# Optimization experiments

Measured on AMD Instinct MI355X. Metric: run time of the kernel, lower is better.

## Reference

```python
import jax, jax.numpy as jnp
import numpy as np

BS, SEQ = 32, 48
VOCAB, H, IMG_F = 32529, 512, 4096
EPS = 1e-5


def setup_inputs() -> dict:
    key = jax.random.key(0)
    ks = jax.random.split(key, 24)
    stdv = 1.0 / np.sqrt(H)
    u = lambda k, shp, s=stdv: jax.random.uniform(k, shp, jnp.float32, -s, s)
    inp = {
        'img': jax.random.normal(ks[0], (BS, IMG_F), jnp.float32),
        'x': jax.random.randint(ks[1], (BS, SEQ), 0, VOCAB),
        # CNN (all convs are kernel-size-1 -> plain linears)
        'w1': u(ks[2], (2048, IMG_F)), 'b1': u(ks[3], (2048,)),
        'g1': jnp.ones((2048,)), 'be1': jnp.zeros((2048,)),
        'w2': u(ks[4], (1024, 2048)), 'b2': u(ks[5], (1024,)),
        'g2': jnp.ones((1024,)), 'be2': jnp.zeros((1024,)),
        'w3': u(ks[6], (H, 1024)), 'b3': u(ks[7], (H,)),
        'g3': jnp.ones((H,)), 'be3': jnp.zeros((H,)),
        # LSTM gates stacked in order i, f, g(c), o
        'U': u(ks[8], (H, 4 * H)),
        'V': u(ks[9], (H, 4 * H)),
        'bg': u(ks[10], (4 * H,)),
        'emb': u(ks[11], (VOCAB, H)),
        'Wout': u(ks[12], (H, VOCAB)),
        'bout': u(ks[13], (VOCAB,)),
    }
    return inp


def _bn(h, g, b):
    # BatchNorm1d in training mode over batch dim (spatial length is 1)
    mu = h.mean(0)
    v = jnp.var(h, 0)
    return g * (h - mu) * jax.lax.rsqrt(v + EPS) + b


def _cnn(img, w1, b1, g1, be1, w2, b2, g2, be2, w3, b3, g3, be3):
    h = jax.nn.relu(_bn(img @ w1.T + b1, g1, be1))
    h = jax.nn.relu(_bn(h @ w2.T + b2, g2, be2))
    h = jax.nn.relu(_bn(h @ w3.T + b3, g3, be3))
    return h  # [bs, 512]


def _lstm(feat, xe, U, V, bg):
    bs = feat.shape[0]
    h = jnp.zeros((bs, H), feat.dtype)
    c = jnp.zeros((bs, H), feat.dtype)

    def gates(z, c):
        z = z.reshape(bs, 4, H)
        i = jax.nn.sigmoid(z[:, 0])
        f = jax.nn.sigmoid(z[:, 1])
        g = jnp.tanh(z[:, 2])
        o = jax.nn.sigmoid(z[:, 3])
        c = f * c + i * g
        return o * jnp.tanh(c), c

    # image step: feat is added identically to every gate pre-activation
    z0 = feat[:, None, :].repeat(4, 1).reshape(bs, 4 * H) + h @ V + bg
    h, c = gates(z0, c)

    # precompute all input projections in one GEMM: [seq, bs, 4H]
    xU = jnp.einsum('bsh,hk->sbk', xe, U)

    def step(carry, xu):
        h, c = carry
        h, c = gates(xu + h @ V + bg, c)
        return (h, c), h

    (h, c), hs = jax.lax.scan(step, (h, c), xU)
    return hs.transpose(1, 0, 2), h, c  # [bs, seq, H]


def reference(img, x, w1, b1, g1, be1, w2, b2, g2, be2, w3, b3, g3, be3,
              U, V, bg, emb, Wout, bout):
    feat = _cnn(img, w1, b1, g1, be1, w2, b2, g2, be2, w3, b3, g3, be3)
    xe = emb[x]  # [bs, seq, H]
    hs, h, c = _lstm(feat, xe, U, V, bg)
    logits = hs @ Wout + bout  # [bs, seq, vocab]
    seq_pred = jax.nn.softmax(logits, axis=2)
    return seq_pred, (h, c)
```

## Files before the change

kernel.cpp:

```cpp
#include <hip/hip_runtime.h>
#include <stdint.h>

#define BS 32
#define SEQ 48
#define VOCAB 32529
#define HD 512
#define IMG_F 4096
#define EPS 1e-5f

typedef __attribute__((ext_vector_type(8))) short short8;
typedef __attribute__((ext_vector_type(4))) float f32x4;

#define MFMA(a, b, c) __builtin_amdgcn_mfma_f32_16x16x32_bf16(a, b, c, 0, 0, 0)

static __device__ __forceinline__ unsigned short f2bf(float v) {
  union { float f; unsigned u; } c; c.f = v;
  unsigned r = (c.u + 0x7FFFu + ((c.u >> 16) & 1u)) >> 16;
  return (unsigned short)r;
}
static __device__ __forceinline__ float bf2f(unsigned short h) {
  union { unsigned u; float f; } c; c.u = ((unsigned)h) << 16; return c.f;
}
static __device__ __forceinline__ float sigf(float x) {
  x = fminf(fmaxf(x, -30.f), 30.f);
  return 1.f / (1.f + __expf(-x));
}
static __device__ __forceinline__ float tanh_(float x) {
  float t = __expf(fminf(fmaxf(2.f * x, -30.f), 30.f));
  return (t - 1.f) / (t + 1.f);
}

__global__ __launch_bounds__(256) void k_gather(const float* __restrict__ emb,
                                                const int* __restrict__ x,
                                                unsigned short* __restrict__ xh,
                                                unsigned short* __restrict__ xl) {
  int idx = blockIdx.x * 256 + threadIdx.x;
  int m = idx >> 7;
  int k4 = (idx & 127) << 2;
  int t = m >> 5, b = m & 31;
  int row = x[b * SEQ + t];
  float4 v = *(const float4*)(emb + (size_t)row * HD + k4);
  float vv[4] = {v.x, v.y, v.z, v.w};
  unsigned short h_[4], l_[4];
#pragma unroll
  for (int i = 0; i < 4; ++i) {
    h_[i] = f2bf(vv[i]);
    l_[i] = f2bf(vv[i] - bf2f(h_[i]));
  }
  ushort4 hq = {h_[0], h_[1], h_[2], h_[3]};
  ushort4 lq = {l_[0], l_[1], l_[2], l_[3]};
  *(ushort4*)(xh + (size_t)m * HD + k4) = hq;
  *(ushort4*)(xl + (size_t)m * HD + k4) = lq;
}

__global__ __launch_bounds__(256) void k_pack(const float* __restrict__ W,
                                              unsigned short* __restrict__ Ph,
                                              unsigned short* __restrict__ Pl) {
  int f = blockIdx.x * 256 + threadIdx.x;
  int lane = f & 63;
  int kk = (f >> 6) & 15;
  int n16 = f >> 10;
  int c = n16 * 16 + (lane & 15);
  int k0 = kk * 32 + (lane >> 4) * 8;
  short8 oh, ol;
#pragma unroll
  for (int i = 0; i < 8; ++i) {
    float v = W[(size_t)(k0 + i) * 2048 + c];
    unsigned short hb = f2bf(v);
    oh[i] = (short)hb;
    ol[i] = (short)f2bf(v - bf2f(hb));
  }
  *(short8*)(Ph + (size_t)f * 8) = oh;
  *(short8*)(Pl + (size_t)f * 8) = ol;
}

template <int INF, int OUTF>
__global__ __launch_bounds__(256) void k_cnn(const float* __restrict__ in,
                                             const float* __restrict__ W,
                                             const float* __restrict__ gamma,
                                             const float* __restrict__ beta,
                                             float* __restrict__ out) {
  int tid = threadIdx.x;
  int b = tid & 31;
  int o = blockIdx.x * 8 + (tid >> 5);
  const float4* ip = (const float4*)(in + (size_t)b * INF);
  const float4* wp = (const float4*)(W + (size_t)o * INF);
  float a0 = 0, a1 = 0, a2 = 0, a3 = 0;
#pragma unroll 4
  for (int k = 0; k < INF / 4; ++k) {
    float4 a = ip[k], w = wp[k];
    a0 = fmaf(a.x, w.x, a0);
    a1 = fmaf(a.y, w.y, a1);
    a2 = fmaf(a.z, w.z, a2);
    a3 = fmaf(a.w, w.w, a3);
  }
  float pre = (a0 + a1) + (a2 + a3);
  float s = pre, q = pre * pre;
#pragma unroll
  for (int mk = 16; mk >= 1; mk >>= 1) {
    s += __shfl_xor(s, mk);
    q += __shfl_xor(q, mk);
  }
  float mu = s * (1.f / 32.f);
  float var = q * (1.f / 32.f) - mu * mu;
  float y = gamma[o] * (pre - mu) * rsqrtf(var + EPS) + beta[o];
  out[(size_t)b * OUTF + o] = fmaxf(y, 0.f);
}

__global__ __launch_bounds__(256) void k_xu(const unsigned short* __restrict__ xh,
                                            const unsigned short* __restrict__ xl,
                                            const unsigned short* __restrict__ Uh,
                                            const unsigned short* __restrict__ Ul,
                                            const float* __restrict__ bg,
                                            float* __restrict__ zx) {
  int mb = blockIdx.x;
  int nb = blockIdx.y;
  int w = threadIdx.x >> 6, l = threadIdx.x & 63;
  int lr = l & 15, lg = l >> 4;
  f32x4 acc[2][2] = {};
#pragma unroll 2
  for (int kk = 0; kk < 16; ++kk) {
    short8 ah[2], al[2];
#pragma unroll
    for (int m = 0; m < 2; ++m) {
      size_t ao = (size_t)(mb * 32 + m * 16 + lr) * HD + kk * 32 + lg * 8;
      ah[m] = *(const short8*)(xh + ao);
      al[m] = *(const short8*)(xl + ao);
    }
#pragma unroll
    for (int n = 0; n < 2; ++n) {
      int n16 = nb * 8 + w * 2 + n;
      size_t bo = ((size_t)(n16 * 16 + kk) * 64 + l) * 8;
      short8 bh = *(const short8*)(Uh + bo);
      short8 bl = *(const short8*)(Ul + bo);
#pragma unroll
      for (int m = 0; m < 2; ++m) {
        acc[m][n] = MFMA(ah[m], bh, acc[m][n]);
        acc[m][n] = MFMA(al[m], bh, acc[m][n]);
        acc[m][n] = MFMA(ah[m], bl, acc[m][n]);
      }
    }
  }
#pragma unroll
  for (int m = 0; m < 2; ++m)
#pragma unroll
    for (int n = 0; n < 2; ++n) {
      int col = (nb * 8 + w * 2 + n) * 16 + lr;
#pragma unroll
      for (int r = 0; r < 4; ++r) {
        int row = mb * 32 + m * 16 + lg * 4 + r;
        zx[(size_t)row * 2048 + col] = acc[m][n][r] + bg[col];
      }
    }
}

__global__ __launch_bounds__(256) void k_step0(const float* __restrict__ feat,
                                               const float* __restrict__ bg,
                                               float* __restrict__ hbuf, float* __restrict__ cbuf,
                                               unsigned short* __restrict__ hh,
                                               unsigned short* __restrict__ hl) {
  int idx = blockIdx.x * 256 + threadIdx.x;
  int j = idx & 511;
  float fv = feat[idx];
  float ig = sigf(fv + bg[j]);
  float gg = tanh_(fv + bg[1024 + j]);
  float og = sigf(fv + bg[1536 + j]);
  float c = ig * gg;
  float h = og * tanh_(c);
  cbuf[idx] = c;
  hbuf[idx] = h;
  unsigned short hb = f2bf(h);
  hh[idx] = hb;
  hl[idx] = f2bf(h - bf2f(hb));
}

__global__ __launch_bounds__(256) void k_step(int t,
    const unsigned short* __restrict__ hih, const unsigned short* __restrict__ hil,
    unsigned short* __restrict__ hoh, unsigned short* __restrict__ hol,
    const unsigned short* __restrict__ Vh, const unsigned short* __restrict__ Vl,
    const float* __restrict__ zx, float* __restrict__ cbuf, float* __restrict__ hbuf,
    unsigned short* __restrict__ hsb) {
  __shared__ float zsh[4][16][17];
  int nb = blockIdx.x & 31;
  int mh = blockIdx.x >> 5;
  int w = threadIdx.x >> 6, l = threadIdx.x & 63;
  int lr = l & 15, lg = l >> 4;
  f32x4 acc = {};
  int n16 = w * 32 + nb;
#pragma unroll 4
  for (int kk = 0; kk < 16; ++kk) {
    size_t ao = (size_t)(mh * 16 + lr) * HD + kk * 32 + lg * 8;
    short8 ah = *(const short8*)(hih + ao);
    short8 al = *(const short8*)(hil + ao);
    size_t bo = ((size_t)(n16 * 16 + kk) * 64 + l) * 8;
    short8 bh = *(const short8*)(Vh + bo);
    short8 bl = *(const short8*)(Vl + bo);
    acc = MFMA(ah, bh, acc);
    acc = MFMA(al, bh, acc);
    acc = MFMA(ah, bl, acc);
  }
#pragma unroll
  for (int r = 0; r < 4; ++r) zsh[w][lg * 4 + r][lr] = acc[r];
  __syncthreads();
  int bl_ = threadIdx.x >> 4;
  int j = threadIdx.x & 15;
  int b = mh * 16 + bl_;
  int col = nb * 16 + j;
  const float* zr = zx + (size_t)(t * 32 + b) * 2048;
  float zi = zsh[0][bl_][j] + zr[col];
  float zf = zsh[1][bl_][j] + zr[512 + col];
  float zg = zsh[2][bl_][j] + zr[1024 + col];
  float zo = zsh[3][bl_][j] + zr[1536 + col];
  float ig = sigf(zi), fg = sigf(zf), gg = tanh_(zg), og = sigf(zo);
  int ci = b * HD + col;
  float c = fg * cbuf[ci] + ig * gg;
  float h = og * tanh_(c);
  cbuf[ci] = c;
  hbuf[ci] = h;
  unsigned short hb = f2bf(h);
  hoh[ci] = hb;
  hol[ci] = f2bf(h - bf2f(hb));
  hsb[((size_t)b * SEQ + t) * HD + col] = hb;
}

template <int MODE>
__global__ __launch_bounds__(256) void k_out(const unsigned short* __restrict__ hsb,
                                             const float* __restrict__ Wout,
                                             const float* __restrict__ bout,
                                             float* __restrict__ rowsum,
                                             float* __restrict__ dst) {
  __shared__ __align__(16) unsigned short Bl[4][64][8];
  int nb = blockIdx.x, mb = blockIdx.y;
  int n0 = nb * 64;
  int tid = threadIdx.x;
  int w = tid >> 6, l = tid & 63, lr = l & 15, lg = l >> 4;
  int mrow0 = mb * 256 + w * 64;
  f32x4 acc[4][4] = {};
  int kl = tid >> 3;
  int nl = (tid & 7) * 8;
  int nsub = nl >> 4;
  int lbase = (nl & 15) | ((kl >> 3) << 4);
  int ifr = kl & 7;
  for (int kk = 0; kk < 16; ++kk) {
    float v[8];
    const float* src = Wout + (size_t)(kk * 32 + kl) * VOCAB + n0 + nl;
#pragma unroll
    for (int i = 0; i < 8; ++i) {
      int gv = n0 + nl + i;
      v[i] = (gv < VOCAB) ? src[i] : 0.f;
    }
    __syncthreads();
#pragma unroll
    for (int i = 0; i < 8; ++i) Bl[nsub][lbase + i][ifr] = f2bf(v[i]);
    __syncthreads();
    short8 a[4];
#pragma unroll
    for (int mt = 0; mt < 4; ++mt)
      a[mt] = *(const short8*)(hsb + (size_t)(mrow0 + mt * 16 + lr) * HD + kk * 32 + lg * 8);
#pragma unroll
    for (int nt = 0; nt < 4; ++nt) {
      short8 bf = *(const short8*)(&Bl[nt][l][0]);
#pragma unroll
      for (int mt = 0; mt < 4; ++mt) acc[mt][nt] = MFMA(a[mt], bf, acc[mt][nt]);
    }
  }
#pragma unroll
  for (int mt = 0; mt < 4; ++mt) {
#pragma unroll
    for (int r = 0; r < 4; ++r) {
      int row = mrow0 + mt * 16 + lg * 4 + r;
      float inv = 1.f;
      if (MODE == 1) inv = 1.f / rowsum[row];
      float s = 0.f;
#pragma unroll
      for (int nt = 0; nt < 4; ++nt) {
        int col = n0 + nt * 16 + lr;
        bool valid = col < VOCAB;
        float logit = acc[mt][nt][r] + (valid ? bout[col] : 0.f);
        float e = __expf(logit);
        if (MODE == 0) {
          s += valid ? e : 0.f;
        } else if (MODE == 2) {
          s += valid ? e : 0.f;
          if (valid) dst[(size_t)row * VOCAB + col] = e;
        } else {
          if (valid) dst[(size_t)row * VOCAB + col] = e * inv;
        }
      }
      if (MODE != 1) {
        s += __shfl_xor(s, 1);
        s += __shfl_xor(s, 2);
        s += __shfl_xor(s, 4);
        s += __shfl_xor(s, 8);
        if (lr == 0) atomicAdd(&rowsum[row], s);
      }
    }
  }
}

__global__ __launch_bounds__(256) void k_div(const float* __restrict__ expb,
                                             const float* __restrict__ rowsum,
                                             float* __restrict__ out) {
  unsigned idx = blockIdx.x * 256u + threadIdx.x;
  unsigned row = idx / (unsigned)VOCAB;
  out[idx] = expb[idx] / rowsum[row];
}

extern "C" void kernel_launch(void* const* d_in, const int* in_sizes, int n_in,
                              void* d_out, int out_size, void* d_ws, size_t ws_size,
                              hipStream_t stream) {
  const float* img  = (const float*)d_in[0];
  const int*   x    = (const int*)d_in[1];
  const float* w1   = (const float*)d_in[2];
  const float* g1   = (const float*)d_in[4];
  const float* be1  = (const float*)d_in[5];
  const float* w2   = (const float*)d_in[6];
  const float* g2   = (const float*)d_in[8];
  const float* be2  = (const float*)d_in[9];
  const float* w3   = (const float*)d_in[10];
  const float* g3   = (const float*)d_in[12];
  const float* be3  = (const float*)d_in[13];
  const float* U    = (const float*)d_in[14];
  const float* V    = (const float*)d_in[15];
  const float* bg   = (const float*)d_in[16];
  const float* emb  = (const float*)d_in[17];
  const float* Wout = (const float*)d_in[18];
  const float* bout = (const float*)d_in[19];

  char* ws = (char*)d_ws;
  size_t off = 0;
  auto alloc = [&](size_t bytes) -> void* {
    void* p = ws + off;
    off = (off + bytes + 255) & ~(size_t)255;
    return p;
  };
  float* zx = (float*)alloc((size_t)48 * 32 * 2048 * 4);
  unsigned short* xh = (unsigned short*)alloc((size_t)1536 * 512 * 2);
  unsigned short* xl = (unsigned short*)alloc((size_t)1536 * 512 * 2);
  unsigned short* Uh = (unsigned short*)alloc((size_t)512 * 2048 * 2);
  unsigned short* Ul = (unsigned short*)alloc((size_t)512 * 2048 * 2);
  unsigned short* Vh = (unsigned short*)alloc((size_t)512 * 2048 * 2);
  unsigned short* Vl = (unsigned short*)alloc((size_t)512 * 2048 * 2);
  unsigned short* hAh = (unsigned short*)alloc(32 * 512 * 2);
  unsigned short* hAl = (unsigned short*)alloc(32 * 512 * 2);
  unsigned short* hBh = (unsigned short*)alloc(32 * 512 * 2);
  unsigned short* hBl = (unsigned short*)alloc(32 * 512 * 2);
  float* hbuf = (float*)alloc(32 * 512 * 4);
  float* cbuf = (float*)alloc(32 * 512 * 4);
  unsigned short* hsb = (unsigned short*)alloc((size_t)1536 * 512 * 2);
  float* feat = (float*)alloc(32 * 512 * 4);
  float* h1 = (float*)alloc(32 * 2048 * 4);
  float* h2 = (float*)alloc(32 * 1024 * 4);
  float* rowsum = (float*)alloc(1536 * 4);
  size_t base = off;
  float* expb = (float*)(ws + base);
  const size_t EXPB = (size_t)49964544 * 4;
  bool onepass = (ws_size >= base + EXPB);

  float* out = (float*)d_out;

  k_gather<<<dim3(768), dim3(256), 0, stream>>>(emb, x, xh, xl);
  k_pack<<<dim3(512), dim3(256), 0, stream>>>(U, Uh, Ul);
  k_pack<<<dim3(512), dim3(256), 0, stream>>>(V, Vh, Vl);
  k_cnn<4096, 2048><<<dim3(256), dim3(256), 0, stream>>>(img, w1, g1, be1, h1);
  k_cnn<2048, 1024><<<dim3(128), dim3(256), 0, stream>>>(h1, w2, g2, be2, h2);
  k_cnn<1024, 512><<<dim3(64), dim3(256), 0, stream>>>(h2, w3, g3, be3, feat);
  k_xu<<<dim3(48, 16), dim3(256), 0, stream>>>(xh, xl, Uh, Ul, bg, zx);
  k_step0<<<dim3(64), dim3(256), 0, stream>>>(feat, bg, hbuf, cbuf, hAh, hAl);
  for (int t = 0; t < 48; ++t) {
    const unsigned short* ih = (t & 1) ? hBh : hAh;
    const unsigned short* il = (t & 1) ? hBl : hAl;
    unsigned short* oh = (t & 1) ? hAh : hBh;
    unsigned short* ol = (t & 1) ? hAl : hBl;
    k_step<<<dim3(64), dim3(256), 0, stream>>>(t, ih, il, oh, ol, Vh, Vl, zx, cbuf, hbuf, hsb);
  }
  hipMemsetAsync(rowsum, 0, 1536 * 4, stream);
  if (onepass) {
    k_out<2><<<dim3(509, 6), dim3(256), 0, stream>>>(hsb, Wout, bout, rowsum, expb);
    k_div<<<dim3(195174), dim3(256), 0, stream>>>(expb, rowsum, out);
  } else {
    k_out<0><<<dim3(509, 6), dim3(256), 0, stream>>>(hsb, Wout, bout, rowsum, out);
    k_out<1><<<dim3(509, 6), dim3(256), 0, stream>>>(hsb, Wout, bout, rowsum, out);
  }
  hipMemcpyAsync(out + 49964544, hbuf, 32 * 512 * 4, hipMemcpyDeviceToDevice, stream);
  hipMemcpyAsync(out + 49964544 + 16384, cbuf, 32 * 512 * 4, hipMemcpyDeviceToDevice, stream);
}
```

Before: 1.502 ms.

## Persistent LSTM kernel with grid barrier, prepacked bf16 Wout, two-pass softmax

Replaces the 48 per-step LSTM launches with one persistent 64-block kernel. It keeps V fragments in registers and synchronises steps with an atomic-counter grid barrier, and writes h/c straight to the output. Wout is prepacked once into an MFMA-ready bf16 layout, so the output GEMM reads B fragments from global memory with no LDS staging or per-tile conversion. The one-pass exp-buffer-plus-divide path is dropped in favour of always running two GEMM passes (sum, then normalise), which recomputes the GEMM but avoids a 200MB intermediate. The grid barrier relies on all 64 blocks being co-resident, and the packing kernel adds its own cost.

```diff
diff --git a/kernel.cpp b/kernel.cpp
--- a/kernel.cpp
+++ b/kernel.cpp
@@ -7,6 +7,7 @@
 #define HD 512
 #define IMG_F 4096
 #define EPS 1e-5f
+#define NPAD16 2040
 
 typedef __attribute__((ext_vector_type(8))) short short8;
 typedef __attribute__((ext_vector_type(4))) float f32x4;
@@ -28,6 +29,17 @@
 static __device__ __forceinline__ float tanh_(float x) {
   float t = __expf(fminf(fmaxf(2.f * x, -30.f), 30.f));
   return (t - 1.f) / (t + 1.f);
+}
+
+static __device__ __forceinline__ void gbar(unsigned* ctr, unsigned target) {
+  __syncthreads();
+  if (threadIdx.x == 0) {
+    __threadfence();
+    atomicAdd(ctr, 1u);
+    while (atomicAdd(ctr, 0u) < target) __builtin_amdgcn_s_sleep(2);
+  }
+  __syncthreads();
+  __threadfence();
 }
 
 __global__ __launch_bounds__(256) void k_gather(const float* __restrict__ emb,
@@ -74,6 +86,23 @@
   *(short8*)(Pl + (size_t)f * 8) = ol;
 }
 
+__global__ __launch_bounds__(256) void k_packw(const float* __restrict__ W,
+                                               unsigned short* __restrict__ P) {
+  int f = blockIdx.x * 256 + threadIdx.x;
+  int lane = f & 63;
+  int kk = (f >> 6) & 15;
+  int n16 = f >> 10;
+  int c = n16 * 16 + (lane & 15);
+  int k0 = kk * 32 + (lane >> 4) * 8;
+  short8 o;
+#pragma unroll
+  for (int i = 0; i < 8; ++i) {
+    float v = (c < VOCAB) ? W[(size_t)(k0 + i) * VOCAB + c] : 0.f;
+    o[i] = (short)f2bf(v);
+  }
+  *(short8*)(P + (size_t)f * 8) = o;
+}
+
 template <int INF, int OUTF>
 __global__ __launch_bounds__(256) void k_cnn(const float* __restrict__ in,
                                              const float* __restrict__ W,
@@ -86,7 +115,7 @@
   const float4* ip = (const float4*)(in + (size_t)b * INF);
   const float4* wp = (const float4*)(W + (size_t)o * INF);
   float a0 = 0, a1 = 0, a2 = 0, a3 = 0;
-#pragma unroll 4
+#pragma unroll 8
   for (int k = 0; k < INF / 4; ++k) {
     float4 a = ip[k], w = wp[k];
     a0 = fmaf(a.x, w.x, a0);
@@ -154,115 +183,111 @@
     }
 }
 
-__global__ __launch_bounds__(256) void k_step0(const float* __restrict__ feat,
-                                               const float* __restrict__ bg,
-                                               float* __restrict__ hbuf, float* __restrict__ cbuf,
-                                               unsigned short* __restrict__ hh,
-                                               unsigned short* __restrict__ hl) {
-  int idx = blockIdx.x * 256 + threadIdx.x;
-  int j = idx & 511;
-  float fv = feat[idx];
-  float ig = sigf(fv + bg[j]);
-  float gg = tanh_(fv + bg[1024 + j]);
-  float og = sigf(fv + bg[1536 + j]);
-  float c = ig * gg;
-  float h = og * tanh_(c);
-  cbuf[idx] = c;
-  hbuf[idx] = h;
-  unsigned short hb = f2bf(h);
-  hh[idx] = hb;
-  hl[idx] = f2bf(h - bf2f(hb));
-}
-
-__global__ __launch_bounds__(256) void k_step(int t,
-    const unsigned short* __restrict__ hih, const unsigned short* __restrict__ hil,
-    unsigned short* __restrict__ hoh, unsigned short* __restrict__ hol,
+__global__ __launch_bounds__(256, 1) void k_lstm(
+    const float* __restrict__ feat, const float* __restrict__ bg,
+    const float* __restrict__ zx,
     const unsigned short* __restrict__ Vh, const unsigned short* __restrict__ Vl,
-    const float* __restrict__ zx, float* __restrict__ cbuf, float* __restrict__ hbuf,
-    unsigned short* __restrict__ hsb) {
+    unsigned short* __restrict__ hAh, unsigned short* __restrict__ hAl,
+    unsigned short* __restrict__ hBh, unsigned short* __restrict__ hBl,
+    unsigned short* __restrict__ hsb, float* __restrict__ hout,
+    float* __restrict__ cout_, unsigned* __restrict__ barctr) {
   __shared__ float zsh[4][16][17];
-  int nb = blockIdx.x & 31;
-  int mh = blockIdx.x >> 5;
-  int w = threadIdx.x >> 6, l = threadIdx.x & 63;
-  int lr = l & 15, lg = l >> 4;
-  f32x4 acc = {};
+  int blk = blockIdx.x;
+  int mh = blk >> 5, nb = blk & 31;
+  int tid = threadIdx.x;
+  int w = tid >> 6, l = tid & 63, lr = l & 15, lg = l >> 4;
   int n16 = w * 32 + nb;
-#pragma unroll 4
+  short8 vh[16], vl[16];
+#pragma unroll
   for (int kk = 0; kk < 16; ++kk) {
-    size_t ao = (size_t)(mh * 16 + lr) * HD + kk * 32 + lg * 8;
-    short8 ah = *(const short8*)(hih + ao);
-    short8 al = *(const short8*)(hil + ao);
     size_t bo = ((size_t)(n16 * 16 + kk) * 64 + l) * 8;
-    short8 bh = *(const short8*)(Vh + bo);
-    short8 bl = *(const short8*)(Vl + bo);
-    acc = MFMA(ah, bh, acc);
-    acc = MFMA(al, bh, acc);
-    acc = MFMA(ah, bl, acc);
-  }
-#pragma unroll
-  for (int r = 0; r < 4; ++r) zsh[w][lg * 4 + r][lr] = acc[r];
-  __syncthreads();
-  int bl_ = threadIdx.x >> 4;
-  int j = threadIdx.x & 15;
-  int b = mh * 16 + bl_;
-  int col = nb * 16 + j;
-  const float* zr = zx + (size_t)(t * 32 + b) * 2048;
-  float zi = zsh[0][bl_][j] + zr[col];
-  float zf = zsh[1][bl_][j] + zr[512 + col];
-  float zg = zsh[2][bl_][j] + zr[1024 + col];
-  float zo = zsh[3][bl_][j] + zr[1536 + col];
-  float ig = sigf(zi), fg = sigf(zf), gg = tanh_(zg), og = sigf(zo);
+    vh[kk] = *(const short8*)(Vh + bo);
+    vl[kk] = *(const short8*)(Vl + bo);
+  }
+  int bl_ = tid >> 4, j = tid & 15;
+  int b = mh * 16 + bl_, col = nb * 16 + j;
   int ci = b * HD + col;
-  float c = fg * cbuf[ci] + ig * gg;
-  float h = og * tanh_(c);
-  cbuf[ci] = c;
-  hbuf[ci] = h;
-  unsigned short hb = f2bf(h);
-  hoh[ci] = hb;
-  hol[ci] = f2bf(h - bf2f(hb));
-  hsb[((size_t)b * SEQ + t) * HD + col] = hb;
+  float fv = feat[ci];
+  float c = sigf(fv + bg[col]) * tanh_(fv + bg[1024 + col]);
+  float h = sigf(fv + bg[1536 + col]) * tanh_(c);
+  {
+    unsigned short hb_ = f2bf(h);
+    hAh[ci] = hb_;
+    hAl[ci] = f2bf(h - bf2f(hb_));
+  }
+  gbar(barctr, 64u);
+  for (int t = 0; t < 48; ++t) {
+    const unsigned short* ih = (t & 1) ? hBh : hAh;
+    const unsigned short* il = (t & 1) ? hBl : hAl;
+    unsigned short* oh = (t & 1) ? hAh : hBh;
+    unsigned short* ol = (t & 1) ? hAl : hBl;
+    const float* zr = zx + ((size_t)t * 32 + b) * 2048 + col;
+    float z0p = zr[0], z1p = zr[512], z2p = zr[1024], z3p = zr[1536];
+    f32x4 acc0 = {}, acc1 = {};
+#pragma unroll
+    for (int kk = 0; kk < 16; ++kk) {
+      size_t ao = (size_t)(mh * 16 + lr) * HD + kk * 32 + lg * 8;
+      short8 ah = *(const short8*)(ih + ao);
+      short8 al = *(const short8*)(il + ao);
+      if (kk & 1) {
+        acc1 = MFMA(ah, vh[kk], acc1);
+        acc1 = MFMA(al, vh[kk], acc1);
+        acc1 = MFMA(ah, vl[kk], acc1);
+      } else {
+        acc0 = MFMA(ah, vh[kk], acc0);
+        acc0 = MFMA(al, vh[kk], acc0);
+        acc0 = MFMA(ah, vl[kk], acc0);
+      }
+    }
+    f32x4 acc;
+#pragma unroll
+    for (int r = 0; r < 4; ++r) acc[r] = acc0[r] + acc1[r];
+#pragma unroll
+    for (int r = 0; r < 4; ++r) zsh[w][lg * 4 + r][lr] = acc[r];
+    __syncthreads();
+    float zi = zsh[0][bl_][j] + z0p;
+    float zf = zsh[1][bl_][j] + z1p;
+    float zg = zsh[2][bl_][j] + z2p;
+    float zo = zsh[3][bl_][j] + z3p;
+    c = sigf(zf) * c + sigf(zi) * tanh_(zg);
+    h = sigf(zo) * tanh_(c);
+    unsigned short hb2 = f2bf(h);
+    oh[ci] = hb2;
+    ol[ci] = f2bf(h - bf2f(hb2));
+    hsb[((size_t)b * SEQ + t) * HD + col] = hb2;
+    if (t < 47) gbar(barctr, 64u * (t + 2));
+  }
+  hout[ci] = h;
+  cout_[ci] = c;
 }
 
 template <int MODE>
-__global__ __launch_bounds__(256) void k_out(const unsigned short* __restrict__ hsb,
-                                             const float* __restrict__ Wout,
+__global__ __launch_bounds__(256) void k_out(const unsigned short* __restrict__ A,
+                                             const unsigned short* __restrict__ B,
                                              const float* __restrict__ bout,
                                              float* __restrict__ rowsum,
                                              float* __restrict__ dst) {
-  __shared__ __align__(16) unsigned short Bl[4][64][8];
-  int nb = blockIdx.x, mb = blockIdx.y;
-  int n0 = nb * 64;
+  int nb = blockIdx.x;
+  int mb = blockIdx.y;
   int tid = threadIdx.x;
   int w = tid >> 6, l = tid & 63, lr = l & 15, lg = l >> 4;
-  int mrow0 = mb * 256 + w * 64;
+  int wr = w >> 1, wc = w & 1;
+  int mrow0 = mb * 128 + wr * 64;
+  int n16_0 = nb * 8 + wc * 4;
   f32x4 acc[4][4] = {};
-  int kl = tid >> 3;
-  int nl = (tid & 7) * 8;
-  int nsub = nl >> 4;
-  int lbase = (nl & 15) | ((kl >> 3) << 4);
-  int ifr = kl & 7;
+#pragma unroll 2
   for (int kk = 0; kk < 16; ++kk) {
-    float v[8];
-    const float* src = Wout + (size_t)(kk * 32 + kl) * VOCAB + n0 + nl;
-#pragma unroll
-    for (int i = 0; i < 8; ++i) {
-      int gv = n0 + nl + i;
-      v[i] = (gv < VOCAB) ? src[i] : 0.f;
-    }
-    __syncthreads();
-#pragma unroll
-    for (int i = 0; i < 8; ++i) Bl[nsub][lbase + i][ifr] = f2bf(v[i]);
-    __syncthreads();
-    short8 a[4];
+    short8 a[4], bf[4];
 #pragma unroll
     for (int mt = 0; mt < 4; ++mt)
-      a[mt] = *(const short8*)(hsb + (size_t)(mrow0 + mt * 16 + lr) * HD + kk * 32 + lg * 8);
-#pragma unroll
-    for (int nt = 0; nt < 4; ++nt) {
-      short8 bf = *(const short8*)(&Bl[nt][l][0]);
-#pragma unroll
-      for (int mt = 0; mt < 4; ++mt) acc[mt][nt] = MFMA(a[mt], bf, acc[mt][nt]);
-    }
+      a[mt] = *(const short8*)(A + (size_t)(mrow0 + mt * 16 + lr) * HD + kk * 32 + lg * 8);
+#pragma unroll
+    for (int nt = 0; nt < 4; ++nt)
+      bf[nt] = *(const short8*)(B + ((size_t)((n16_0 + nt) * 16 + kk) * 64 + l) * 8);
+#pragma unroll
+    for (int nt = 0; nt < 4; ++nt)
+#pragma unroll
+      for (int mt = 0; mt < 4; ++mt) acc[mt][nt] = MFMA(a[mt], bf[nt], acc[mt][nt]);
   }
 #pragma unroll
   for (int mt = 0; mt < 4; ++mt) {
@@ -274,20 +299,16 @@
       float s = 0.f;
 #pragma unroll
       for (int nt = 0; nt < 4; ++nt) {
-        int col = n0 + nt * 16 + lr;
+        int col = (n16_0 + nt) * 16 + lr;
         bool valid = col < VOCAB;
-        float logit = acc[mt][nt][r] + (valid ? bout[col] : 0.f);
-        float e = __expf(logit);
+        float e = __expf(acc[mt][nt][r] + (valid ? bout[col] : 0.f));
         if (MODE == 0) {
           s += valid ? e : 0.f;
-        } else if (MODE == 2) {
-          s += valid ? e : 0.f;
-          if (valid) dst[(size_t)row * VOCAB + col] = e;
         } else {
           if (valid) dst[(size_t)row * VOCAB + col] = e * inv;
         }
       }
-      if (MODE != 1) {
+      if (MODE == 0) {
         s += __shfl_xor(s, 1);
         s += __shfl_xor(s, 2);
         s += __shfl_xor(s, 4);
@@ -296,14 +317,6 @@
       }
     }
   }
-}
-
-__global__ __launch_bounds__(256) void k_div(const float* __restrict__ expb,
-                                             const float* __restrict__ rowsum,
-                                             float* __restrict__ out) {
-  unsigned idx = blockIdx.x * 256u + threadIdx.x;
-  unsigned row = idx / (unsigned)VOCAB;
-  out[idx] = expb[idx] / rowsum[row];
 }
 
 extern "C" void kernel_launch(void* const* d_in, const int* in_sizes, int n_in,
@@ -341,47 +354,34 @@
   unsigned short* Ul = (unsigned short*)alloc((size_t)512 * 2048 * 2);
   unsigned short* Vh = (unsigned short*)alloc((size_t)512 * 2048 * 2);
   unsigned short* Vl = (unsigned short*)alloc((size_t)512 * 2048 * 2);
+  unsigned short* Wp = (unsigned short*)alloc((size_t)NPAD16 * 16 * 64 * 8 * 2);
   unsigned short* hAh = (unsigned short*)alloc(32 * 512 * 2);
   unsigned short* hAl = (unsigned short*)alloc(32 * 512 * 2);
   unsigned short* hBh = (unsigned short*)alloc(32 * 512 * 2);
   unsigned short* hBl = (unsigned short*)alloc(32 * 512 * 2);
-  float* hbuf = (float*)alloc(32 * 512 * 4);
-  float* cbuf = (float*)alloc(32 * 512 * 4);
   unsigned short* hsb = (unsigned short*)alloc((size_t)1536 * 512 * 2);
   float* feat = (float*)alloc(32 * 512 * 4);
   float* h1 = (float*)alloc(32 * 2048 * 4);
   float* h2 = (float*)alloc(32 * 1024 * 4);
   float* rowsum = (float*)alloc(1536 * 4);
-  size_t base = off;
-  float* expb = (float*)(ws + base);
-  const size_t EXPB = (size_t)49964544 * 4;
-  bool onepass = (ws_size >= base + EXPB);
+  unsigned* barctr = (unsigned*)alloc(256);
 
   float* out = (float*)d_out;
+  float* hout = out + 49964544;
+  float* cout_ = out + 49964544 + 16384;
 
   k_gather<<<dim3(768), dim3(256), 0, stream>>>(emb, x, xh, xl);
   k_pack<<<dim3(512), dim3(256), 0, stream>>>(U, Uh, Ul);
   k_pack<<<dim3(512), dim3(256), 0, stream>>>(V, Vh, Vl);
+  k_packw<<<dim3(8160), dim3(256), 0, stream>>>(Wout, Wp);
   k_cnn<4096, 2048><<<dim3(256), dim3(256), 0, stream>>>(img, w1, g1, be1, h1);
   k_cnn<2048, 1024><<<dim3(128), dim3(256), 0, stream>>>(h1, w2, g2, be2, h2);
   k_cnn<1024, 512><<<dim3(64), dim3(256), 0, stream>>>(h2, w3, g3, be3, feat);
   k_xu<<<dim3(48, 16), dim3(256), 0, stream>>>(xh, xl, Uh, Ul, bg, zx);
-  k_step0<<<dim3(64), dim3(256), 0, stream>>>(feat, bg, hbuf, cbuf, hAh, hAl);
-  for (int t = 0; t < 48; ++t) {
-    const unsigned short* ih = (t & 1) ? hBh : hAh;
-    const unsigned short* il = (t & 1) ? hBl : hAl;
-    unsigned short* oh = (t & 1) ? hAh : hBh;
-    unsigned short* ol = (t & 1) ? hAl : hBl;
-    k_step<<<dim3(64), dim3(256), 0, stream>>>(t, ih, il, oh, ol, Vh, Vl, zx, cbuf, hbuf, hsb);
-  }
+  hipMemsetAsync(barctr, 0, 256, stream);
   hipMemsetAsync(rowsum, 0, 1536 * 4, stream);
-  if (onepass) {
-    k_out<2><<<dim3(509, 6), dim3(256), 0, stream>>>(hsb, Wout, bout, rowsum, expb);
-    k_div<<<dim3(195174), dim3(256), 0, stream>>>(expb, rowsum, out);
-  } else {
-    k_out<0><<<dim3(509, 6), dim3(256), 0, stream>>>(hsb, Wout, bout, rowsum, out);
-    k_out<1><<<dim3(509, 6), dim3(256), 0, stream>>>(hsb, Wout, bout, rowsum, out);
-  }
-  hipMemcpyAsync(out + 49964544, hbuf, 32 * 512 * 4, hipMemcpyDeviceToDevice, stream);
-  hipMemcpyAsync(out + 49964544 + 16384, cbuf, 32 * 512 * 4, hipMemcpyDeviceToDevice, stream);
-}
+  k_lstm<<<dim3(64), dim3(256), 0, stream>>>(feat, bg, zx, Vh, Vl, hAh, hAl, hBh, hBl,
+                                             hsb, hout, cout_, barctr);
+  k_out<0><<<dim3(255, 12), dim3(256), 0, stream>>>(hsb, Wp, bout, rowsum, out);
+  k_out<1><<<dim3(255, 12), dim3(256), 0, stream>>>(hsb, Wp, bout, rowsum, out);
+}
```

Result: slower. 1.662 ms (+10.7%).
